# Performance work log

Measured on AMD Instinct MI355X. Metric: run time of the kernel, lower is better.

Reference implementation:

```python
import jax, jax.numpy as jnp
import numpy as np

SHAPE = (192, 192, 192)


def _trilinear_sample(img, z, y, x):
    # img: [B,C,D,H,W]; z,y,x: [B,D,H,W] absolute voxel coords (align_corners=True,
    # zero padding outside the volume, matching F.grid_sample defaults in vroc).
    B, C, D, H, W = img.shape
    imgf = img.reshape(B, C, -1)
    z0 = jnp.floor(z); y0 = jnp.floor(y); x0 = jnp.floor(x)
    wz = z - z0; wy = y - y0; wx = x - x0
    z0i = z0.astype(jnp.int32); y0i = y0.astype(jnp.int32); x0i = x0.astype(jnp.int32)
    z1i = z0i + 1; y1i = y0i + 1; x1i = x0i + 1

    def gather(iz, iy, ix):
        valid = ((iz >= 0) & (iz < D) & (iy >= 0) & (iy < H) & (ix >= 0) & (ix < W))
        lin = ((jnp.clip(iz, 0, D - 1) * H + jnp.clip(iy, 0, H - 1)) * W
               + jnp.clip(ix, 0, W - 1)).reshape(B, 1, -1)
        v = jnp.take_along_axis(imgf, jnp.broadcast_to(lin, (B, C, D * H * W)), axis=2)
        return v.reshape(B, C, D, H, W) * valid.reshape(B, 1, D, H, W).astype(img.dtype)

    def w(a, b, c):
        return (a * b * c)[:, None]  # [B,1,D,H,W]

    out = (gather(z0i, y0i, x0i) * w(1 - wz, 1 - wy, 1 - wx)
           + gather(z0i, y0i, x1i) * w(1 - wz, 1 - wy, wx)
           + gather(z0i, y1i, x0i) * w(1 - wz, wy, 1 - wx)
           + gather(z0i, y1i, x1i) * w(1 - wz, wy, wx)
           + gather(z1i, y0i, x0i) * w(wz, 1 - wy, 1 - wx)
           + gather(z1i, y0i, x1i) * w(wz, 1 - wy, wx)
           + gather(z1i, y1i, x0i) * w(wz, wy, 1 - wx)
           + gather(z1i, y1i, x1i) * w(wz, wy, wx))
    return out


def _warp(moving_image, vector_field):
    # SpatialTransformer: identity grid + displacement (voxel units), trilinear sample.
    B, C, D, H, W = moving_image.shape
    dt = moving_image.dtype
    gz, gy, gx = jnp.meshgrid(jnp.arange(D, dtype=dt), jnp.arange(H, dtype=dt),
                              jnp.arange(W, dtype=dt), indexing='ij')
    z = gz[None] + vector_field[:, 0]
    y = gy[None] + vector_field[:, 1]
    x = gx[None] + vector_field[:, 2]
    return _trilinear_sample(moving_image, z, y, x)


def setup_inputs() -> dict:
    key = jax.random.key(0)
    k1, k2, k3, k4 = jax.random.split(key, 4)
    D, H, W = SHAPE
    moving_image = jax.random.normal(k1, (1, 1, D, H, W), dtype=jnp.float32)
    vector_field = jax.random.normal(k2, (1, 3, D, H, W), dtype=jnp.float32) * 3.0
    fixed_image = jax.random.normal(k3, (1, 1, D, H, W), dtype=jnp.float32)
    fixed_image_mask = jax.random.randint(k4, (1, 1, D, H, W), 0, 2).astype(bool)
    return {"moving_image": moving_image, "vector_field": vector_field,
            "fixed_image": fixed_image, "fixed_image_mask": fixed_image_mask}


def reference(moving_image, vector_field, fixed_image, fixed_image_mask):
    warped = _warp(moving_image, vector_field)
    m = fixed_image_mask.astype(warped.dtype)
    sq = (warped - fixed_image) ** 2
    # F.mse_loss(warped[mask], fixed[mask]) == mean of squared diff over masked voxels
    return jnp.sum(sq * m) / jnp.maximum(jnp.sum(m), 1.0)
```

## Files before the change

kernel.cpp:

```cpp
#include <hip/hip_runtime.h>
#include <hip/hip_fp16.h>

#define DD 192
#define HH 192
#define WW 192
#define NVOX (DD * HH * WW)

#define RSX 32
#define RSY 33
#define RSZ 33
#define ROWD 16
#define SLABD (RSY * ROWD)
#define RTOTH (RSX * RSY * RSZ)
#define RTOTD (RTOTH / 2)
#define NCHUNK (RTOTH / 8)
#define CHSLAB (RSY * 4)
#define NT 1024
#define GRID 256

#define AS1 __attribute__((address_space(1)))
#define AS3 __attribute__((address_space(3)))

__global__ __launch_bounds__(256) void conv_fp16(
    const float4* __restrict__ in, int4* __restrict__ out)
{
    const int i = blockIdx.x * 256 + threadIdx.x;
    const float4 a = in[2 * i];
    const float4 b = in[2 * i + 1];
    __half2 h0 = __floats2half2_rn(a.x, a.y);
    __half2 h1 = __floats2half2_rn(a.z, a.w);
    __half2 h2 = __floats2half2_rn(b.x, b.y);
    __half2 h3 = __floats2half2_rn(b.z, b.w);
    int4 o;
    o.x = *(int*)&h0; o.y = *(int*)&h1; o.z = *(int*)&h2; o.w = *(int*)&h3;
    out[i] = o;
}

struct Streams { float4 dz, dy, dx, f; int4 m; };

__device__ __forceinline__ void tile_coords(int n, int& tx, int& ty, int& tz) {
    tx = n / 144;
    const int r = n - tx * 144;
    ty = r / 12;
    tz = r - ty * 12;
}

__device__ __forceinline__ void stage_tile(
    const ushort* __restrict__ movh, const ushort* __restrict__ zbuf,
    uint* sbufd, int x_lo, int y_lo, int z_lo, int tid)
{
    ushort* sbuf = (ushort*)sbufd;
    #pragma unroll
    for (int i = 0; i < 5; ++i) {
        const int q = tid + i * NT;
        if (q < NCHUNK) {
            const int rz = q / CHSLAB;
            const int rem = q - rz * CHSLAB;
            const int ry = rem >> 2;
            const int k  = rem & 3;
            const int gz = z_lo + rz, gy = y_lo + ry, gx = x_lo + 8 * k;
            const bool valid = ((unsigned)gz < DD) & ((unsigned)gy < HH) &
                               ((unsigned)gx < WW);
            const ushort* src = valid ? (movh + ((gz * HH + gy) * WW + gx)) : zbuf;
            const int qb = i * NT + (tid & ~63);
            __builtin_amdgcn_global_load_lds((AS1 void*)src,
                                             (AS3 void*)(sbuf + 8 * qb), 16, 0, 0);
        }
    }
}

__device__ __forceinline__ Streams prefetch_streams(
    const float* __restrict__ vf, const float* __restrict__ fix,
    const int* __restrict__ mask, int base)
{
    Streams s;
    s.dz = *(const float4*)(vf + base);
    s.dy = *(const float4*)(vf + NVOX + base);
    s.dx = *(const float4*)(vf + 2 * NVOX + base);
    s.f  = *(const float4*)(fix + base);
    s.m  = *(const int4*)(mask + base);
    return s;
}

__global__ __launch_bounds__(NT) void warp_mse_persist(
    const ushort* __restrict__ movh,
    const float* __restrict__ mov,
    const float* __restrict__ vf,
    const float* __restrict__ fix,
    const int* __restrict__ mask,
    const ushort* __restrict__ zbuf,
    float* __restrict__ acc,
    float* __restrict__ out)
{
    __shared__ uint sbufd[2][RTOTD];
    __shared__ float s_sq[16], s_cnt[16];

    const int tid = threadIdx.x;
    const int b = blockIdx.x;
    const int start = b * 6 + min(b, 192);
    const int cnt_t = 6 + (b < 192 ? 1 : 0);

    const int lxg = (tid & 3) * 4;
    const int ly  = (tid >> 2) & 15;
    const int lz  = tid >> 6;

    float sq = 0.0f, cntm = 0.0f;

    int tx, ty, tz;
    tile_coords(start, tx, ty, tz);
    stage_tile(movh, zbuf, sbufd[0], tx * 16 - 8, ty * 16 - 8, tz * 16 - 8, tid);
    Streams S0 = prefetch_streams(vf, fix, mask,
        ((tz * 16 + lz) * HH + ty * 16 + ly) * WW + tx * 16 + lxg);
    __syncthreads();

    for (int k = 0; k < cnt_t; ++k) {
        const int cur = k & 1;
        Streams S1 = S0;
        if (k + 1 < cnt_t) {
            int nx, ny, nz;
            tile_coords(start + k + 1, nx, ny, nz);
            stage_tile(movh, zbuf, sbufd[cur ^ 1],
                       nx * 16 - 8, ny * 16 - 8, nz * 16 - 8, tid);
            S1 = prefetch_streams(vf, fix, mask,
                ((nz * 16 + lz) * HH + ny * 16 + ly) * WW + nx * 16 + lxg);
        }

        int cx, cy, cz;
        tile_coords(start + k, cx, cy, cz);
        const int x_lo = cx * 16 - 8, y_lo = cy * 16 - 8, z_lo = cz * 16 - 8;
        const int gz = cz * 16 + lz, gy = cy * 16 + ly, gx0 = cx * 16 + lxg;
        const uint* sdw = sbufd[cur];

        uint fbmask = 0;

        auto proc = [&](float dz, float dy, float dx, float f, int m, int j) {
            const float z = (float)gz + dz, y = (float)gy + dy,
                        x = (float)(gx0 + j) + dx;
            const float z0f = floorf(z), y0f = floorf(y), x0f = floorf(x);
            const float wz = z - z0f, wy = y - y0f, wx = x - x0f;
            const int z0 = (int)z0f, y0 = (int)y0f, x0 = (int)x0f;
            const int z0l = z0 - z_lo, y0l = y0 - y_lo, x0l = x0 - x_lo;
            const bool inbox = ((unsigned)z0l < RSZ - 1) &
                               ((unsigned)y0l < RSY - 1) &
                               ((unsigned)x0l < RSX - 1);
            if (inbox) {
                const int o = z0l * SLABD + y0l * ROWD + (x0l >> 1);
                const bool odd = (x0l & 1) != 0;
                const uint a00 = sdw[o];
                const uint b00 = sdw[o + 1];
                const uint a01 = sdw[o + ROWD];
                const uint b01 = sdw[o + ROWD + 1];
                const uint a10 = sdw[o + SLABD];
                const uint b10 = sdw[o + SLABD + 1];
                const uint a11 = sdw[o + SLABD + ROWD];
                const uint b11 = sdw[o + SLABD + ROWD + 1];
                float v000, v001, v010, v011, v100, v101, v110, v111;
                auto pr = [&](uint A, uint B, float& l, float& r) {
                    const float2 fa = __half22float2(*(const __half2*)&A);
                    const float fb = __low2float(*(const __half2*)&B);
                    l = odd ? fa.y : fa.x;
                    r = odd ? fb   : fa.y;
                };
                pr(a00, b00, v000, v001);
                pr(a01, b01, v010, v011);
                pr(a10, b10, v100, v101);
                pr(a11, b11, v110, v111);
                const float c00 = v000 + (v001 - v000) * wx;
                const float c01 = v010 + (v011 - v010) * wx;
                const float c10 = v100 + (v101 - v100) * wx;
                const float c11 = v110 + (v111 - v110) * wx;
                const float c0 = c00 + (c01 - c00) * wy;
                const float c1 = c10 + (c11 - c10) * wy;
                const float warped = c0 + (c1 - c0) * wz;
                const float mm = (m != 0) ? 1.0f : 0.0f;
                const float diff = warped - f;
                sq += diff * diff * mm;
                cntm += mm;
            } else {
                fbmask |= (1u << j);
            }
        };
        proc(S0.dz.x, S0.dy.x, S0.dx.x, S0.f.x, S0.m.x, 0);
        proc(S0.dz.y, S0.dy.y, S0.dx.y, S0.f.y, S0.m.y, 1);
        proc(S0.dz.z, S0.dy.z, S0.dx.z, S0.f.z, S0.m.z, 2);
        proc(S0.dz.w, S0.dy.w, S0.dx.w, S0.f.w, S0.m.w, 3);

        if (__builtin_expect(fbmask != 0, 0)) {
            auto fb = [&](float dz, float dy, float dx, float f, int m, int j) {
                if (!(fbmask & (1u << j))) return;
                const float z = (float)gz + dz, y = (float)gy + dy,
                            x = (float)(gx0 + j) + dx;
                const float z0f = floorf(z), y0f = floorf(y), x0f = floorf(x);
                const float wz = z - z0f, wy = y - y0f, wx = x - x0f;
                const int z0 = (int)z0f, y0 = (int)y0f, x0 = (int)x0f;
                const int z1 = z0 + 1, y1 = y0 + 1, x1 = x0 + 1;
                const bool zi0 = (unsigned)z0 < DD, zi1 = (unsigned)z1 < DD;
                const bool yi0 = (unsigned)y0 < HH, yi1 = (unsigned)y1 < HH;
                const bool xi0 = (unsigned)x0 < WW, xi1 = (unsigned)x1 < WW;
                auto ld = [&](int iz, int iy, int ix, bool ok) -> float {
                    return ok ? mov[(iz * HH + iy) * WW + ix] : 0.0f;
                };
                const float v000 = ld(z0, y0, x0, zi0 & yi0 & xi0);
                const float v001 = ld(z0, y0, x1, zi0 & yi0 & xi1);
                const float v010 = ld(z0, y1, x0, zi0 & yi1 & xi0);
                const float v011 = ld(z0, y1, x1, zi0 & yi1 & xi1);
                const float v100 = ld(z1, y0, x0, zi1 & yi0 & xi0);
                const float v101 = ld(z1, y0, x1, zi1 & yi0 & xi1);
                const float v110 = ld(z1, y1, x0, zi1 & yi1 & xi0);
                const float v111 = ld(z1, y1, x1, zi1 & yi1 & xi1);
                const float c00 = v000 + (v001 - v000) * wx;
                const float c01 = v010 + (v011 - v010) * wx;
                const float c10 = v100 + (v101 - v100) * wx;
                const float c11 = v110 + (v111 - v110) * wx;
                const float c0 = c00 + (c01 - c00) * wy;
                const float c1 = c10 + (c11 - c10) * wy;
                const float warped = c0 + (c1 - c0) * wz;
                const float mm = (m != 0) ? 1.0f : 0.0f;
                const float diff = warped - f;
                sq += diff * diff * mm;
                cntm += mm;
            };
            fb(S0.dz.x, S0.dy.x, S0.dx.x, S0.f.x, S0.m.x, 0);
            fb(S0.dz.y, S0.dy.y, S0.dx.y, S0.f.y, S0.m.y, 1);
            fb(S0.dz.z, S0.dy.z, S0.dx.z, S0.f.z, S0.m.z, 2);
            fb(S0.dz.w, S0.dy.w, S0.dx.w, S0.f.w, S0.m.w, 3);
        }

        __syncthreads();
        S0 = S1;
    }

    #pragma unroll
    for (int off = 32; off > 0; off >>= 1) {
        sq   += __shfl_down(sq, off, 64);
        cntm += __shfl_down(cntm, off, 64);
    }
    const int lane = tid & 63;
    const int wid = tid >> 6;
    if (lane == 0) { s_sq[wid] = sq; s_cnt[wid] = cntm; }
    __syncthreads();
    if (tid == 0) {
        float bsq = 0.0f, bcnt = 0.0f;
        #pragma unroll
        for (int i = 0; i < 16; ++i) { bsq += s_sq[i]; bcnt += s_cnt[i]; }
        atomicAdd(&acc[0], bsq);
        atomicAdd(&acc[1], bcnt);
        __threadfence();
        const unsigned old = atomicAdd((unsigned*)&acc[2], 1u);
        if (old == GRID - 1) {
            __threadfence();
            const float s = atomicAdd(&acc[0], 0.0f);
            const float c = atomicAdd(&acc[1], 0.0f);
            out[0] = s / fmaxf(c, 1.0f);
        }
    }
}

__global__ __launch_bounds__(256) void warp_mse_simple(
    const float* __restrict__ mov, const float* __restrict__ vf,
    const float* __restrict__ fix, const int* __restrict__ mask,
    float* __restrict__ acc)
{
    const int idx = blockIdx.x * 256 + threadIdx.x;
    float sq = 0.0f, cnt = 0.0f;
    if (idx < NVOX) {
        const int w = idx % WW;
        const int t = idx / WW;
        const int h = t % HH;
        const int d = t / HH;
        const float z = (float)d + vf[idx];
        const float y = (float)h + vf[NVOX + idx];
        const float x = (float)w + vf[2 * NVOX + idx];
        const float z0f = floorf(z), y0f = floorf(y), x0f = floorf(x);
        const float wz = z - z0f, wy = y - y0f, wx = x - x0f;
        const int z0 = (int)z0f, y0 = (int)y0f, x0 = (int)x0f;
        const int z1 = z0 + 1, y1 = y0 + 1, x1 = x0 + 1;
        const bool zi0 = (unsigned)z0 < DD, zi1 = (unsigned)z1 < DD;
        const bool yi0 = (unsigned)y0 < HH, yi1 = (unsigned)y1 < HH;
        const bool xi0 = (unsigned)x0 < WW, xi1 = (unsigned)x1 < WW;
        auto ld = [&](int iz, int iy, int ix, bool ok) -> float {
            return ok ? mov[(iz * HH + iy) * WW + ix] : 0.0f;
        };
        const float v000 = ld(z0, y0, x0, zi0 & yi0 & xi0);
        const float v001 = ld(z0, y0, x1, zi0 & yi0 & xi1);
        const float v010 = ld(z0, y1, x0, zi0 & yi1 & xi0);
        const float v011 = ld(z0, y1, x1, zi0 & yi1 & xi1);
        const float v100 = ld(z1, y0, x0, zi1 & yi0 & xi0);
        const float v101 = ld(z1, y0, x1, zi1 & yi0 & xi1);
        const float v110 = ld(z1, y1, x0, zi1 & yi1 & xi0);
        const float v111 = ld(z1, y1, x1, zi1 & yi1 & xi1);
        const float c00 = v000 + (v001 - v000) * wx;
        const float c01 = v010 + (v011 - v010) * wx;
        const float c10 = v100 + (v101 - v100) * wx;
        const float c11 = v110 + (v111 - v110) * wx;
        const float c0 = c00 + (c01 - c00) * wy;
        const float c1 = c10 + (c11 - c10) * wy;
        const float warped = c0 + (c1 - c0) * wz;
        const float m = (mask[idx] != 0) ? 1.0f : 0.0f;
        const float diff = warped - fix[idx];
        sq = diff * diff * m;
        cnt = m;
    }
    #pragma unroll
    for (int off = 32; off > 0; off >>= 1) {
        sq  += __shfl_down(sq, off, 64);
        cnt += __shfl_down(cnt, off, 64);
    }
    __shared__ float s_sq[4], s_cnt[4];
    const int lane = threadIdx.x & 63, wid = threadIdx.x >> 6;
    if (lane == 0) { s_sq[wid] = sq; s_cnt[wid] = cnt; }
    __syncthreads();
    if (threadIdx.x == 0) {
        atomicAdd(&acc[0], s_sq[0] + s_sq[1] + s_sq[2] + s_sq[3]);
        atomicAdd(&acc[1], s_cnt[0] + s_cnt[1] + s_cnt[2] + s_cnt[3]);
    }
}

__global__ void warp_mse_finalize(const float* __restrict__ acc, float* __restrict__ out) {
    out[0] = acc[0] / fmaxf(acc[1], 1.0f);
}

extern "C" void kernel_launch(void* const* d_in, const int* in_sizes, int n_in,
                              void* d_out, int out_size, void* d_ws, size_t ws_size,
                              hipStream_t stream) {
    const float* mov  = (const float*)d_in[0];
    const float* vf   = (const float*)d_in[1];
    const float* fix  = (const float*)d_in[2];
    const int*   mask = (const int*)d_in[3];
    float* acc = (float*)d_ws;
    float* out = (float*)d_out;

    hipMemsetAsync(d_ws, 0, 256, stream);

    const size_t need = 256 + (size_t)NVOX * 2;
    if (ws_size >= need) {
        ushort* movh = (ushort*)((char*)d_ws + 256);
        const ushort* zbuf = (const ushort*)((char*)d_ws + 64);
        conv_fp16<<<NVOX / (256 * 8), 256, 0, stream>>>(
            (const float4*)mov, (int4*)movh);
        warp_mse_persist<<<GRID, NT, 0, stream>>>(movh, mov, vf, fix, mask,
                                                  zbuf, acc, out);
    } else {
        warp_mse_simple<<<(NVOX + 255) / 256, 256, 0, stream>>>(mov, vf, fix, mask, acc);
        warp_mse_finalize<<<1, 1, 0, stream>>>(acc, out);
    }
}
```

Before: 248.1 us.

## Compact out-of-box fallback samples into a shared queue processed by all threads

Voxels whose trilinear footprint falls outside the staged shared-memory box are no longer handled by a divergent per-lane fallback. Each one is appended to a block-wide LDS queue through a shared atomic, and after a barrier all threads drain the queue together using fp16 global loads. The goal is to stop one straggling lane from stalling its whole wavefront on eight scattered global loads. In exchange it adds an extra __syncthreads per tile, LDS atomics, and extra LDS for the queue, which may lower occupancy. It also reads fp16 rather than fp32 values on the fallback path, and any overflow beyond the queue capacity still takes the fp32 inline path.

```diff
diff --git a/kernel.cpp b/kernel.cpp
--- a/kernel.cpp
+++ b/kernel.cpp
@@ -17,6 +17,7 @@
 #define CHSLAB (RSY * 4)
 #define NT 1024
 #define GRID 256
+#define QCAP 512
 
 #define AS1 __attribute__((address_space(1)))
 #define AS3 __attribute__((address_space(3)))
@@ -94,6 +95,9 @@
 {
     __shared__ uint sbufd[2][RTOTD];
     __shared__ float s_sq[16], s_cnt[16];
+    __shared__ unsigned qn[2];
+    __shared__ uint  qp[QCAP];
+    __shared__ float4 qw[QCAP];
 
     const int tid = threadIdx.x;
     const int b = blockIdx.x;
@@ -106,6 +110,7 @@
 
     float sq = 0.0f, cntm = 0.0f;
 
+    if (tid < 2) qn[tid] = 0;
     int tx, ty, tz;
     tile_coords(start, tx, ty, tz);
     stage_tile(movh, zbuf, sbufd[0], tx * 16 - 8, ty * 16 - 8, tz * 16 - 8, tid);
@@ -130,8 +135,6 @@
         const int x_lo = cx * 16 - 8, y_lo = cy * 16 - 8, z_lo = cz * 16 - 8;
         const int gz = cz * 16 + lz, gy = cy * 16 + ly, gx0 = cx * 16 + lxg;
         const uint* sdw = sbufd[cur];
-
-        uint fbmask = 0;
 
         auto proc = [&](float dz, float dy, float dx, float f, int m, int j) {
             const float z = (float)gz + dz, y = (float)gy + dy,
@@ -177,7 +180,42 @@
                 sq += diff * diff * mm;
                 cntm += mm;
             } else {
-                fbmask |= (1u << j);
+                const uint slot = atomicAdd(&qn[cur], 1u);
+                if (slot < QCAP) {
+                    const int px = min(max(x0, -5), 196) + 8;
+                    const int py = min(max(y0, -5), 196) + 8;
+                    const int pz = min(max(z0, -5), 196) + 8;
+                    qp[slot] = (uint)px | ((uint)py << 8) | ((uint)pz << 16) |
+                               ((m != 0) ? 0x80000000u : 0u);
+                    qw[slot] = make_float4(wx, wy, wz, f);
+                } else {
+                    const int z1 = z0 + 1, y1 = y0 + 1, x1 = x0 + 1;
+                    const bool zi0 = (unsigned)z0 < DD, zi1 = (unsigned)z1 < DD;
+                    const bool yi0 = (unsigned)y0 < HH, yi1 = (unsigned)y1 < HH;
+                    const bool xi0 = (unsigned)x0 < WW, xi1 = (unsigned)x1 < WW;
+                    auto ld = [&](int iz, int iy, int ix, bool ok) -> float {
+                        return ok ? mov[(iz * HH + iy) * WW + ix] : 0.0f;
+                    };
+                    const float v000 = ld(z0, y0, x0, zi0 & yi0 & xi0);
+                    const float v001 = ld(z0, y0, x1, zi0 & yi0 & xi1);
+                    const float v010 = ld(z0, y1, x0, zi0 & yi1 & xi0);
+                    const float v011 = ld(z0, y1, x1, zi0 & yi1 & xi1);
+                    const float v100 = ld(z1, y0, x0, zi1 & yi0 & xi0);
+                    const float v101 = ld(z1, y0, x1, zi1 & yi0 & xi1);
+                    const float v110 = ld(z1, y1, x0, zi1 & yi1 & xi0);
+                    const float v111 = ld(z1, y1, x1, zi1 & yi1 & xi1);
+                    const float c00 = v000 + (v001 - v000) * wx;
+                    const float c01 = v010 + (v011 - v010) * wx;
+                    const float c10 = v100 + (v101 - v100) * wx;
+                    const float c11 = v110 + (v111 - v110) * wx;
+                    const float c0 = c00 + (c01 - c00) * wy;
+                    const float c1 = c10 + (c11 - c10) * wy;
+                    const float warped = c0 + (c1 - c0) * wz;
+                    const float mm = (m != 0) ? 1.0f : 0.0f;
+                    const float diff = warped - f;
+                    sq += diff * diff * mm;
+                    cntm += mm;
+                }
             }
         };
         proc(S0.dz.x, S0.dy.x, S0.dx.x, S0.f.x, S0.m.x, 0);
@@ -185,45 +223,44 @@
         proc(S0.dz.z, S0.dy.z, S0.dx.z, S0.f.z, S0.m.z, 2);
         proc(S0.dz.w, S0.dy.w, S0.dx.w, S0.f.w, S0.m.w, 3);
 
-        if (__builtin_expect(fbmask != 0, 0)) {
-            auto fb = [&](float dz, float dy, float dx, float f, int m, int j) {
-                if (!(fbmask & (1u << j))) return;
-                const float z = (float)gz + dz, y = (float)gy + dy,
-                            x = (float)(gx0 + j) + dx;
-                const float z0f = floorf(z), y0f = floorf(y), x0f = floorf(x);
-                const float wz = z - z0f, wy = y - y0f, wx = x - x0f;
-                const int z0 = (int)z0f, y0 = (int)y0f, x0 = (int)x0f;
-                const int z1 = z0 + 1, y1 = y0 + 1, x1 = x0 + 1;
-                const bool zi0 = (unsigned)z0 < DD, zi1 = (unsigned)z1 < DD;
-                const bool yi0 = (unsigned)y0 < HH, yi1 = (unsigned)y1 < HH;
-                const bool xi0 = (unsigned)x0 < WW, xi1 = (unsigned)x1 < WW;
-                auto ld = [&](int iz, int iy, int ix, bool ok) -> float {
-                    return ok ? mov[(iz * HH + iy) * WW + ix] : 0.0f;
-                };
-                const float v000 = ld(z0, y0, x0, zi0 & yi0 & xi0);
-                const float v001 = ld(z0, y0, x1, zi0 & yi0 & xi1);
-                const float v010 = ld(z0, y1, x0, zi0 & yi1 & xi0);
-                const float v011 = ld(z0, y1, x1, zi0 & yi1 & xi1);
-                const float v100 = ld(z1, y0, x0, zi1 & yi0 & xi0);
-                const float v101 = ld(z1, y0, x1, zi1 & yi0 & xi1);
-                const float v110 = ld(z1, y1, x0, zi1 & yi1 & xi0);
-                const float v111 = ld(z1, y1, x1, zi1 & yi1 & xi1);
-                const float c00 = v000 + (v001 - v000) * wx;
-                const float c01 = v010 + (v011 - v010) * wx;
-                const float c10 = v100 + (v101 - v100) * wx;
-                const float c11 = v110 + (v111 - v110) * wx;
-                const float c0 = c00 + (c01 - c00) * wy;
-                const float c1 = c10 + (c11 - c10) * wy;
-                const float warped = c0 + (c1 - c0) * wz;
-                const float mm = (m != 0) ? 1.0f : 0.0f;
-                const float diff = warped - f;
-                sq += diff * diff * mm;
-                cntm += mm;
+        __syncthreads();
+
+        const uint qcount = min(qn[cur], (uint)QCAP);
+        if (tid == 0) qn[cur ^ 1] = 0;
+        for (uint i = tid; i < qcount; i += NT) {
+            const uint pos = qp[i];
+            const float4 w4 = qw[i];
+            const int x0 = (int)(pos & 255u) - 8;
+            const int y0 = (int)((pos >> 8) & 255u) - 8;
+            const int z0 = (int)((pos >> 16) & 255u) - 8;
+            const float mm = (pos & 0x80000000u) ? 1.0f : 0.0f;
+            const int z1 = z0 + 1, y1 = y0 + 1, x1 = x0 + 1;
+            const bool zi0 = (unsigned)z0 < DD, zi1 = (unsigned)z1 < DD;
+            const bool yi0 = (unsigned)y0 < HH, yi1 = (unsigned)y1 < HH;
+            const bool xi0 = (unsigned)x0 < WW, xi1 = (unsigned)x1 < WW;
+            auto ld = [&](int iz, int iy, int ix, bool ok) -> float {
+                return ok ? __half2float(*(const __half*)(movh +
+                                ((iz * HH + iy) * WW + ix))) : 0.0f;
             };
-            fb(S0.dz.x, S0.dy.x, S0.dx.x, S0.f.x, S0.m.x, 0);
-            fb(S0.dz.y, S0.dy.y, S0.dx.y, S0.f.y, S0.m.y, 1);
-            fb(S0.dz.z, S0.dy.z, S0.dx.z, S0.f.z, S0.m.z, 2);
-            fb(S0.dz.w, S0.dy.w, S0.dx.w, S0.f.w, S0.m.w, 3);
+            const float v000 = ld(z0, y0, x0, zi0 & yi0 & xi0);
+            const float v001 = ld(z0, y0, x1, zi0 & yi0 & xi1);
+            const float v010 = ld(z0, y1, x0, zi0 & yi1 & xi0);
+            const float v011 = ld(z0, y1, x1, zi0 & yi1 & xi1);
+            const float v100 = ld(z1, y0, x0, zi1 & yi0 & xi0);
+            const float v101 = ld(z1, y0, x1, zi1 & yi0 & xi1);
+            const float v110 = ld(z1, y1, x0, zi1 & yi1 & xi0);
+            const float v111 = ld(z1, y1, x1, zi1 & yi1 & xi1);
+            const float wx = w4.x, wy = w4.y, wz = w4.z;
+            const float c00 = v000 + (v001 - v000) * wx;
+            const float c01 = v010 + (v011 - v010) * wx;
+            const float c10 = v100 + (v101 - v100) * wx;
+            const float c11 = v110 + (v111 - v110) * wx;
+            const float c0 = c00 + (c01 - c00) * wy;
+            const float c1 = c10 + (c11 - c10) * wy;
+            const float warped = c0 + (c1 - c0) * wz;
+            const float diff = warped - w4.w;
+            sq += diff * diff * mm;
+            cntm += mm;
         }
 
         __syncthreads();
```

After: 249.4 us. Within noise of the previous version (+0.6%).
